# Kernel optimization log

Measured on AMD Instinct MI355X. Metric: run time of the kernel, lower is better.

## Reference

```python
import jax, jax.numpy as jnp
import numpy as np

N_NODES = 50000
NEG_SLOPE = 0.2


def gat_conv(x, W, att_src, att_dst, b, src, dst, n):
    # x: [N, F_in], W: [F_in, H*C], att_*: [H, C], b: [H*C]
    H, C = att_src.shape
    h = (x @ W).reshape(n, H, C)                       # [N, H, C]
    a_s = (h * att_src).sum(-1)                        # [N, H]
    a_d = (h * att_dst).sum(-1)                        # [N, H]
    e = jax.nn.leaky_relu(a_s[src] + a_d[dst], NEG_SLOPE)  # [E, H]
    # segment softmax over destination node (every node has a self-loop)
    m = jax.ops.segment_max(e, dst, num_segments=n)    # [N, H]
    ex = jnp.exp(e - m[dst])
    denom = jax.ops.segment_sum(ex, dst, num_segments=n)
    alpha = ex / denom[dst]                            # [E, H]
    out = jax.ops.segment_sum(alpha[:, :, None] * h[src], dst, num_segments=n)
    return out.reshape(n, H * C) + b


def setup_inputs() -> dict:
    key = jax.random.key(0)
    ks = jax.random.split(key, 10)
    n, e = N_NODES, 1600000
    x = jax.random.normal(ks[0], (n, 128), dtype=jnp.float32)
    edge_index = jax.random.randint(ks[1], (2, e), 0, n, dtype=jnp.int64)
    s = 0.1
    return {
        "x": x,
        "edge_index": edge_index,
        "W1": jax.random.normal(ks[2], (128, 128), dtype=jnp.float32) * s,
        "att_src1": jax.random.normal(ks[3], (4, 32), dtype=jnp.float32) * s,
        "att_dst1": jax.random.normal(ks[4], (4, 32), dtype=jnp.float32) * s,
        "b1": jnp.zeros((128,), dtype=jnp.float32),
        "W2": jax.random.normal(ks[5], (128, 128), dtype=jnp.float32) * s,
        "att_src2": jax.random.normal(ks[6], (4, 32), dtype=jnp.float32) * s,
        "att_dst2": jax.random.normal(ks[7], (4, 32), dtype=jnp.float32) * s,
        "b2": jnp.zeros((128,), dtype=jnp.float32),
    }


def reference(x, edge_index, W1, att_src1, att_dst1, b1, W2, att_src2, att_dst2, b2):
    n = x.shape[0]
    loops = jnp.arange(n, dtype=edge_index.dtype)
    src = jnp.concatenate([edge_index[0], loops])  # add self-loops (PyG default)
    dst = jnp.concatenate([edge_index[1], loops])
    h = gat_conv(x, W1, att_src1, att_dst1, b1, src, dst, n)
    h = jax.nn.relu(h)
    h = gat_conv(h, W2, att_src2, att_dst2, b2, src, dst, n)
    return (h, h)
```

## Files before the change

### kernel.cpp

```cpp
#include <hip/hip_runtime.h>
#include <hip/hip_bf16.h>


#define FDIM 128
#define NHEAD 4
#define NB 512

__device__ inline unsigned short f2bf(float f) {
    union { float f; unsigned u; } v; v.f = f;
    unsigned r = v.u + 0x7fff + ((v.u >> 16) & 1);
    return (unsigned short)(r >> 16);
}
__device__ inline float2 bf2f(unsigned v) {
    union { unsigned u; float f; } a, b;
    a.u = v << 16;
    b.u = v & 0xffff0000u;
    return make_float2(a.f, b.f);
}

__global__ __launch_bounds__(256) void gemm128(const float* __restrict__ A,
                                               const float* __restrict__ B,
                                               unsigned short* __restrict__ C,
                                               const float* __restrict__ att_s,
                                               const float* __restrict__ att_d,
                                               float* __restrict__ a_s,
                                               float* __restrict__ a_d, int M) {
    __shared__ float As[128 * 64];
    __shared__ float Bs[128 * 128];
    const int tid = threadIdx.x;
    const int bm = blockIdx.x * 64;

    #pragma unroll
    for (int i = 0; i < 16; i++) {
        int idx = tid + i * 256;
        ((float4*)Bs)[idx] = ((const float4*)B)[idx];
    }
    #pragma unroll
    for (int i = 0; i < 8; i++) {
        int idx = tid + i * 256;
        int row = idx >> 5;
        int k4  = idx & 31;
        int grow = bm + row;
        float4 v = make_float4(0.f, 0.f, 0.f, 0.f);
        if (grow < M) v = ((const float4*)A)[grow * 32 + k4];
        As[(k4 * 4 + 0) * 64 + row] = v.x;
        As[(k4 * 4 + 1) * 64 + row] = v.y;
        As[(k4 * 4 + 2) * 64 + row] = v.z;
        As[(k4 * 4 + 3) * 64 + row] = v.w;
    }
    __syncthreads();

    const int mg = tid >> 5;
    const int ng = tid & 31;
    float acc[8][4] = {};
    const float* Ap = &As[mg * 8];
    const float* Bp = &Bs[ng * 4];
    #pragma unroll 4
    for (int k = 0; k < 128; k++) {
        float4 a0 = *(const float4*)(Ap + k * 64);
        float4 a1 = *(const float4*)(Ap + k * 64 + 4);
        float4 b  = *(const float4*)(Bp + k * 128);
        float av[8] = {a0.x, a0.y, a0.z, a0.w, a1.x, a1.y, a1.z, a1.w};
        float bv[4] = {b.x, b.y, b.z, b.w};
        #pragma unroll
        for (int i = 0; i < 8; i++)
            #pragma unroll
            for (int j = 0; j < 4; j++)
                acc[i][j] += av[i] * bv[j];
    }

    const float4 atS = ((const float4*)att_s)[ng];
    const float4 atD = ((const float4*)att_d)[ng];
    #pragma unroll
    for (int i = 0; i < 8; i++) {
        int grow = bm + mg * 8 + i;
        float ps = acc[i][0] * atS.x + acc[i][1] * atS.y + acc[i][2] * atS.z + acc[i][3] * atS.w;
        float pd = acc[i][0] * atD.x + acc[i][1] * atD.y + acc[i][2] * atD.z + acc[i][3] * atD.w;
        ps += __shfl_xor(ps, 1, 64); pd += __shfl_xor(pd, 1, 64);
        ps += __shfl_xor(ps, 2, 64); pd += __shfl_xor(pd, 2, 64);
        ps += __shfl_xor(ps, 4, 64); pd += __shfl_xor(pd, 4, 64);
        if (grow < M) {
            ((ushort4*)C)[grow * 32 + ng] =
                make_ushort4(f2bf(acc[i][0]), f2bf(acc[i][1]),
                             f2bf(acc[i][2]), f2bf(acc[i][3]));
            if ((ng & 7) == 0) {
                a_s[grow * NHEAD + (ng >> 3)] = ps;
                a_d[grow * NHEAD + (ng >> 3)] = pd;
            }
        }
    }
}

__global__ __launch_bounds__(256) void bucket_hist(const int* __restrict__ dst, int E,
                                                   unsigned long long magic,
                                                   int* __restrict__ bcnt) {
    __shared__ int sh[NB];
    const int t = threadIdx.x;
    for (int i = t; i < NB; i += 256) sh[i] = 0;
    __syncthreads();
    for (int i = blockIdx.x * blockDim.x + t; i < E; i += gridDim.x * blockDim.x) {
        int b = (int)(((unsigned long long)(unsigned)dst[i] * magic) >> 40);
        atomicAdd(&sh[b], 1);
    }
    __syncthreads();
    for (int i = t; i < NB; i += 256)
        if (sh[i]) atomicAdd(&bcnt[i], sh[i]);
}

__global__ __launch_bounds__(256) void bucket_scan(const int* __restrict__ bcnt,
                                                   int* __restrict__ bbase,
                                                   int* __restrict__ bcursor,
                                                   int* __restrict__ row_ptr,
                                                   int N, int E) {
    __shared__ int wsum[4];
    const int t = threadIdx.x, lane = t & 63, wid = t >> 6;
    int v0 = bcnt[2 * t], v1 = bcnt[2 * t + 1];
    int s = v0 + v1, incl = s;
    #pragma unroll
    for (int o = 1; o < 64; o <<= 1) {
        int u = __shfl_up(incl, o, 64);
        if (lane >= o) incl += u;
    }
    if (lane == 63) wsum[wid] = incl;
    __syncthreads();
    if (t == 0) {
        int a = 0;
        #pragma unroll
        for (int i = 0; i < 4; i++) { int x = wsum[i]; wsum[i] = a; a += x; }
    }
    __syncthreads();
    int excl = wsum[wid] + incl - s;
    bbase[2 * t] = excl;          bcursor[2 * t] = excl;
    bbase[2 * t + 1] = excl + v0; bcursor[2 * t + 1] = excl + v0;
    if (t == 0) { bbase[NB] = E; row_ptr[N] = E; }
}

__global__ __launch_bounds__(256) void partition(const int* __restrict__ src,
                                                 const int* __restrict__ dst, int E,
                                                 unsigned long long magic,
                                                 int* __restrict__ bcursor,
                                                 int2* __restrict__ ebuf) {
    __shared__ int shc[NB];
    __shared__ int shb[NB];
    __shared__ int shcur[NB];
    const int t = threadIdx.x;
    for (int i = t; i < NB; i += 256) shc[i] = 0;
    __syncthreads();
    const int e0 = blockIdx.x * 4096;
    int myb[16], mys[16], myd[16];
    #pragma unroll
    for (int u = 0; u < 16; u++) {
        int i = e0 + u * 256 + t;
        if (i < E) {
            mys[u] = src[i];
            myd[u] = dst[i];
            int b = (int)(((unsigned long long)(unsigned)myd[u] * magic) >> 40);
            myb[u] = b;
            atomicAdd(&shc[b], 1);
        } else myb[u] = -1;
    }
    __syncthreads();
    for (int i = t; i < NB; i += 256) {
        int c = shc[i];
        shcur[i] = 0;
        if (c) shb[i] = atomicAdd(&bcursor[i], c);
    }
    __syncthreads();
    #pragma unroll
    for (int u = 0; u < 16; u++) {
        if (myb[u] >= 0) {
            int o = atomicAdd(&shcur[myb[u]], 1);
            ebuf[shb[myb[u]] + o] = make_int2(mys[u], myd[u]);
        }
    }
}

__global__ __launch_bounds__(256) void build_bucket(const int2* __restrict__ ebuf,
                                                    const int* __restrict__ bbase,
                                                    int npb, int N,
                                                    int* __restrict__ row_ptr,
                                                    int* __restrict__ col) {
    __shared__ int degl[256];
    __shared__ int curl[256];
    const int b = blockIdx.x;
    const int t = threadIdx.x, lane = t & 63, wid = t >> 6;
    const int base = bbase[b];
    const int cnt = bbase[b + 1] - base;
    const int node0 = b * npb;
    for (int i = t; i < npb; i += 256) degl[i] = 0;
    __syncthreads();
    for (int i = t; i < cnt; i += 256) {
        int d = ebuf[base + i].y;
        atomicAdd(&degl[d - node0], 1);
    }
    __syncthreads();
    if (wid == 0) {
        int run = 0;
        for (int c = 0; c * 64 < npb; c++) {
            int idx = c * 64 + lane;
            int v = (idx < npb) ? degl[idx] : 0;
            int incl = v;
            #pragma unroll
            for (int o = 1; o < 64; o <<= 1) {
                int u = __shfl_up(incl, o, 64);
                if (lane >= o) incl += u;
            }
            int excl = incl - v + run;
            if (idx < npb) {
                curl[idx] = excl;
                int node = node0 + idx;
                if (node < N) row_ptr[node] = base + excl;
            }
            run += __shfl(incl, 63, 64);
        }
    }
    __syncthreads();
    for (int i = t; i < cnt; i += 256) {
        int2 ed = ebuf[base + i];
        int p = atomicAdd(&curl[ed.y - node0], 1);
        col[base + p] = ed.x;
    }
}

__global__ __launch_bounds__(64) void aggregate(const unsigned short* __restrict__ h,
                                                const float* __restrict__ a_s,
                                                const float* __restrict__ a_d,
                                                const int* __restrict__ row_ptr,
                                                const int* __restrict__ col,
                                                const float* __restrict__ bias,
                                                float* __restrict__ out,
                                                float* __restrict__ out2,
                                                int n, int do_relu) {
    const int nid = blockIdx.x;
    const int c = threadIdx.x;
    const int hd = c >> 4;
    const float ad = a_d[nid * NHEAD + hd];
    const unsigned* __restrict__ h2 = (const unsigned*)h;

    float e = a_s[nid * NHEAD + hd] + ad;
    e = (e > 0.f) ? e : 0.2f * e;
    float den = __expf(e);
    float2 hv = bf2f(h2[(size_t)nid * 64 + c]);
    float num0 = den * hv.x, num1 = den * hv.y;

    const int beg = row_ptr[nid], end = row_ptr[nid + 1];
    int j = beg;
    for (; j + 8 <= end; j += 8) {
        int s[8];
        #pragma unroll
        for (int u = 0; u < 8; u++) s[u] = col[j + u];
        unsigned v[8]; float el[8];
        #pragma unroll
        for (int u = 0; u < 8; u++) v[u] = h2[(size_t)s[u] * 64 + c];
        #pragma unroll
        for (int u = 0; u < 8; u++) el[u] = a_s[s[u] * NHEAD + hd];
        #pragma unroll
        for (int u = 0; u < 8; u++) {
            float e2 = el[u] + ad;
            e2 = (e2 > 0.f) ? e2 : 0.2f * e2;
            float w = __expf(e2);
            den += w;
            float2 f = bf2f(v[u]);
            num0 += w * f.x;
            num1 += w * f.y;
        }
    }
    for (; j < end; j++) {
        int s = col[j];
        float e2 = a_s[s * NHEAD + hd] + ad;
        e2 = (e2 > 0.f) ? e2 : 0.2f * e2;
        float w = __expf(e2);
        den += w;
        float2 f = bf2f(h2[(size_t)s * 64 + c]);
        num0 += w * f.x;
        num1 += w * f.y;
    }
    float2 bv = ((const float2*)bias)[c];
    float rd = 1.0f / den;
    float o0 = num0 * rd + bv.x;
    float o1 = num1 * rd + bv.y;
    if (do_relu) { o0 = fmaxf(o0, 0.f); o1 = fmaxf(o1, 0.f); }
    ((float2*)out)[(size_t)nid * 64 + c] = make_float2(o0, o1);
    if (out2) ((float2*)out2)[(size_t)nid * 64 + c] = make_float2(o0, o1);
}

extern "C" void kernel_launch(void* const* d_in, const int* in_sizes, int n_in,
                              void* d_out, int out_size, void* d_ws, size_t ws_size,
                              hipStream_t stream) {
    const float* x        = (const float*)d_in[0];
    const int*   edge     = (const int*)d_in[1];
    const float* W1       = (const float*)d_in[2];
    const float* att_s1   = (const float*)d_in[3];
    const float* att_d1   = (const float*)d_in[4];
    const float* b1       = (const float*)d_in[5];
    const float* W2       = (const float*)d_in[6];
    const float* att_s2   = (const float*)d_in[7];
    const float* att_d2   = (const float*)d_in[8];
    const float* b2       = (const float*)d_in[9];
    float* out = (float*)d_out;

    const int N = in_sizes[0] / FDIM;
    const int E = in_sizes[1] / 2;
    const int* src = edge;
    const int* dst = edge + E;

    const int npb = (N + NB - 1) / NB;
    const unsigned long long magic = ((1ull << 40) / (unsigned long long)npb) + 1;

    char* w = (char*)d_ws;
    size_t off = 0;
    auto alloc = [&](size_t bytes) { void* p = w + off; off = (off + bytes + 255) & ~(size_t)255; return p; };
    int*   row_ptr = (int*)alloc((size_t)(N + 1) * 4);
    int*   col     = (int*)alloc((size_t)E * 4);
    int*   bcnt    = (int*)alloc((size_t)NB * 4);
    int*   bbase   = (int*)alloc((size_t)(NB + 1) * 4);
    int*   bcursor = (int*)alloc((size_t)NB * 4);
    unsigned short* h1 = (unsigned short*)alloc((size_t)N * FDIM * 2);
    float* hx      = (float*)alloc((size_t)N * FDIM * 4);
    float* as1     = (float*)alloc((size_t)N * NHEAD * 4);
    float* ad1     = (float*)alloc((size_t)N * NHEAD * 4);
    float* as2     = (float*)alloc((size_t)N * NHEAD * 4);
    float* ad2     = (float*)alloc((size_t)N * NHEAD * 4);
    int2*  ebuf    = (int2*)hx;
    (void)ws_size;

    hipMemsetAsync(bcnt, 0, (size_t)NB * 4, stream);
    bucket_hist<<<1024, 256, 0, stream>>>(dst, E, magic, bcnt);
    bucket_scan<<<1, 256, 0, stream>>>(bcnt, bbase, bcursor, row_ptr, N, E);
    partition<<<(E + 4095) / 4096, 256, 0, stream>>>(src, dst, E, magic, bcursor, ebuf);
    build_bucket<<<NB, 256, 0, stream>>>(ebuf, bbase, npb, N, row_ptr, col);

    const int gblocks = (N + 63) / 64;

    gemm128<<<gblocks, 256, 0, stream>>>(x, W1, h1, att_s1, att_d1, as1, ad1, N);
    aggregate<<<N, 64, 0, stream>>>(h1, as1, ad1, row_ptr, col, b1, hx, nullptr, N, 1);

    gemm128<<<gblocks, 256, 0, stream>>>(hx, W2, h1, att_s2, att_d2, as2, ad2, N);
    aggregate<<<N, 64, 0, stream>>>(h1, as2, ad2, row_ptr, col, b2,
                                    out, out + (size_t)N * FDIM, N, 0);
}
```

Before: 386.3 us.

## Replace FP32 SIMT GEMM with split-bf16 MFMA GEMM and fused attention dots

Replaces the scalar FP32 GEMM with a matrix-core kernel that splits each FP32 operand into bf16 hi and lo parts and issues three MFMA 32x32x16 products to approximate FP32 accuracy. The weights are pre-split and stored in LDS with an XOR swizzle by a small prep kernel, so B loads avoid bank conflicts. The output tile is staged through LDS for coalesced 16-byte stores, and the per-head attention dot products are recomputed there from the bf16 values. This trades slightly different numerics (the attention logits now come from rounded bf16 h) and two extra tiny launches for much higher GEMM throughput. The GEMMs are only part of the total time, which is dominated by graph building and aggregation.

```diff
diff --git a/kernel.cpp b/kernel.cpp
--- a/kernel.cpp
+++ b/kernel.cpp
@@ -5,6 +5,9 @@
 #define FDIM 128
 #define NHEAD 4
 #define NB 512
+
+typedef __attribute__((ext_vector_type(16))) float f32x16;
+typedef __attribute__((ext_vector_type(8)))  short s16x8;
 
 __device__ inline unsigned short f2bf(float f) {
     union { float f; unsigned u; } v; v.f = f;
@@ -18,75 +21,140 @@
     return make_float2(a.f, b.f);
 }
 
-__global__ __launch_bounds__(256) void gemm128(const float* __restrict__ A,
-                                               const float* __restrict__ B,
-                                               unsigned short* __restrict__ C,
-                                               const float* __restrict__ att_s,
-                                               const float* __restrict__ att_d,
-                                               float* __restrict__ a_s,
-                                               float* __restrict__ a_d, int M) {
-    __shared__ float As[128 * 64];
-    __shared__ float Bs[128 * 128];
-    const int tid = threadIdx.x;
+__global__ __launch_bounds__(256) void prep_w(const float* __restrict__ W,
+                                              short* __restrict__ Bhi,
+                                              short* __restrict__ Blo) {
+    const int t = threadIdx.x;
+    for (int i = 0; i < 64; i++) {
+        int e = i * 256 + t;
+        int k = e >> 7, n = e & 127;
+        float f = W[e];
+        unsigned u = __float_as_uint(f);
+        unsigned short hi = (unsigned short)(u >> 16);
+        float rem = f - __uint_as_float(u & 0xffff0000u);
+        unsigned short lo = (unsigned short)(__float_as_uint(rem) >> 16);
+        int idx = n * 128 + ((((k >> 3) ^ (n & 15))) << 3) + (k & 7);
+        Bhi[idx] = (short)hi;
+        Blo[idx] = (short)lo;
+    }
+}
+
+__global__ __launch_bounds__(256) void gemm_mfma(const float* __restrict__ A,
+                                                 const short* __restrict__ Bghi,
+                                                 const short* __restrict__ Bglo,
+                                                 unsigned short* __restrict__ H,
+                                                 const float* __restrict__ att_s,
+                                                 const float* __restrict__ att_d,
+                                                 float* __restrict__ a_s,
+                                                 float* __restrict__ a_d, int M) {
+    __shared__ short Bsm[2][16384];
+    __shared__ float attsm[256];
+    const int t = threadIdx.x;
     const int bm = blockIdx.x * 64;
 
-    #pragma unroll
-    for (int i = 0; i < 16; i++) {
-        int idx = tid + i * 256;
-        ((float4*)Bs)[idx] = ((const float4*)B)[idx];
-    }
-    #pragma unroll
-    for (int i = 0; i < 8; i++) {
-        int idx = tid + i * 256;
-        int row = idx >> 5;
-        int k4  = idx & 31;
-        int grow = bm + row;
-        float4 v = make_float4(0.f, 0.f, 0.f, 0.f);
-        if (grow < M) v = ((const float4*)A)[grow * 32 + k4];
-        As[(k4 * 4 + 0) * 64 + row] = v.x;
-        As[(k4 * 4 + 1) * 64 + row] = v.y;
-        As[(k4 * 4 + 2) * 64 + row] = v.z;
-        As[(k4 * 4 + 3) * 64 + row] = v.w;
-    }
-    __syncthreads();
-
-    const int mg = tid >> 5;
-    const int ng = tid & 31;
-    float acc[8][4] = {};
-    const float* Ap = &As[mg * 8];
-    const float* Bp = &Bs[ng * 4];
-    #pragma unroll 4
-    for (int k = 0; k < 128; k++) {
-        float4 a0 = *(const float4*)(Ap + k * 64);
-        float4 a1 = *(const float4*)(Ap + k * 64 + 4);
-        float4 b  = *(const float4*)(Bp + k * 128);
-        float av[8] = {a0.x, a0.y, a0.z, a0.w, a1.x, a1.y, a1.z, a1.w};
-        float bv[4] = {b.x, b.y, b.z, b.w};
-        #pragma unroll
-        for (int i = 0; i < 8; i++)
+    if (t < 128) attsm[t] = att_s[t];
+    else         attsm[t] = att_d[t - 128];
+
+    {
+        const uint4* ghi = (const uint4*)Bghi;
+        const uint4* glo = (const uint4*)Bglo;
+        uint4* shi = (uint4*)&Bsm[0][0];
+        uint4* slo = (uint4*)&Bsm[1][0];
+        #pragma unroll
+        for (int i = 0; i < 8; i++) {
+            shi[t + i * 256] = ghi[t + i * 256];
+            slo[t + i * 256] = glo[t + i * 256];
+        }
+    }
+
+    const int lane = t & 63;
+    const int w = t >> 6;
+    const int wr = w >> 1, wc = w & 1;
+    const int m  = lane & 31, h2 = lane >> 5;
+    const int grow = bm + wr * 32 + m;
+
+    s16x8 ahi[8], alo[8];
+    {
+        const bool ok = grow < M;
+        const float* ap = A + (size_t)grow * 128 + 8 * h2;
+        #pragma unroll
+        for (int c = 0; c < 8; c++) {
+            float ff[8];
+            if (ok) {
+                float4 f0 = *(const float4*)(ap + c * 16);
+                float4 f1 = *(const float4*)(ap + c * 16 + 4);
+                ff[0]=f0.x; ff[1]=f0.y; ff[2]=f0.z; ff[3]=f0.w;
+                ff[4]=f1.x; ff[5]=f1.y; ff[6]=f1.z; ff[7]=f1.w;
+            } else {
+                #pragma unroll
+                for (int j = 0; j < 8; j++) ff[j] = 0.f;
+            }
             #pragma unroll
-            for (int j = 0; j < 4; j++)
-                acc[i][j] += av[i] * bv[j];
-    }
-
-    const float4 atS = ((const float4*)att_s)[ng];
-    const float4 atD = ((const float4*)att_d)[ng];
-    #pragma unroll
-    for (int i = 0; i < 8; i++) {
-        int grow = bm + mg * 8 + i;
-        float ps = acc[i][0] * atS.x + acc[i][1] * atS.y + acc[i][2] * atS.z + acc[i][3] * atS.w;
-        float pd = acc[i][0] * atD.x + acc[i][1] * atD.y + acc[i][2] * atD.z + acc[i][3] * atD.w;
-        ps += __shfl_xor(ps, 1, 64); pd += __shfl_xor(pd, 1, 64);
-        ps += __shfl_xor(ps, 2, 64); pd += __shfl_xor(pd, 2, 64);
-        ps += __shfl_xor(ps, 4, 64); pd += __shfl_xor(pd, 4, 64);
-        if (grow < M) {
-            ((ushort4*)C)[grow * 32 + ng] =
-                make_ushort4(f2bf(acc[i][0]), f2bf(acc[i][1]),
-                             f2bf(acc[i][2]), f2bf(acc[i][3]));
-            if ((ng & 7) == 0) {
-                a_s[grow * NHEAD + (ng >> 3)] = ps;
-                a_d[grow * NHEAD + (ng >> 3)] = pd;
+            for (int j = 0; j < 8; j++) {
+                unsigned u = __float_as_uint(ff[j]);
+                float rem = ff[j] - __uint_as_float(u & 0xffff0000u);
+                ahi[c][j] = (short)(u >> 16);
+                alo[c][j] = (short)(__float_as_uint(rem) >> 16);
             }
+        }
+    }
+    __syncthreads();
+
+    f32x16 acc[2];
+    #pragma unroll
+    for (int i = 0; i < 16; i++) { acc[0][i] = 0.f; acc[1][i] = 0.f; }
+
+    #pragma unroll
+    for (int ni = 0; ni < 2; ni++) {
+        const int n = ni * 64 + wc * 32 + m;
+        const int nbase = n * 128;
+        #pragma unroll
+        for (int c = 0; c < 8; c++) {
+            int chunk8 = 2 * c + h2;
+            int koff = ((chunk8 ^ (n & 15)) << 3);
+            s16x8 bhi = *(const s16x8*)&Bsm[0][nbase + koff];
+            s16x8 blo = *(const s16x8*)&Bsm[1][nbase + koff];
+            acc[ni] = __builtin_amdgcn_mfma_f32_32x32x16_bf16(ahi[c], bhi, acc[ni], 0, 0, 0);
+            acc[ni] = __builtin_amdgcn_mfma_f32_32x32x16_bf16(alo[c], bhi, acc[ni], 0, 0, 0);
+            acc[ni] = __builtin_amdgcn_mfma_f32_32x32x16_bf16(ahi[c], blo, acc[ni], 0, 0, 0);
+        }
+    }
+
+    __syncthreads();
+    unsigned short* htile = (unsigned short*)&Bsm[0][0];
+    #pragma unroll
+    for (int ni = 0; ni < 2; ni++) {
+        const int colg = ni * 64 + wc * 32 + m;
+        #pragma unroll
+        for (int r = 0; r < 16; r++) {
+            int row = wr * 32 + (r & 3) + 8 * (r >> 2) + 4 * h2;
+            htile[row * 128 + colg] = (short)f2bf(acc[ni][r]);
+        }
+    }
+    __syncthreads();
+
+    {
+        const int r = t >> 2, q = t & 3;
+        const int growr = bm + r;
+        if (growr < M) {
+            uint4 v0 = *(uint4*)&htile[r * 128 + q * 32];
+            uint4 v1 = *(uint4*)&htile[r * 128 + q * 32 + 8];
+            uint4 v2 = *(uint4*)&htile[r * 128 + q * 32 + 16];
+            uint4 v3 = *(uint4*)&htile[r * 128 + q * 32 + 24];
+            uint4* hg = (uint4*)(H + (size_t)growr * 128);
+            hg[q * 4 + 0] = v0; hg[q * 4 + 1] = v1;
+            hg[q * 4 + 2] = v2; hg[q * 4 + 3] = v3;
+            unsigned uu[16] = {v0.x, v0.y, v0.z, v0.w, v1.x, v1.y, v1.z, v1.w,
+                               v2.x, v2.y, v2.z, v2.w, v3.x, v3.y, v3.z, v3.w};
+            float ps = 0.f, pd = 0.f;
+            #pragma unroll
+            for (int i = 0; i < 16; i++) {
+                float2 f = bf2f(uu[i]);
+                ps += f.x * attsm[q * 32 + 2 * i]       + f.y * attsm[q * 32 + 2 * i + 1];
+                pd += f.x * attsm[128 + q * 32 + 2 * i] + f.y * attsm[128 + q * 32 + 2 * i + 1];
+            }
+            a_s[growr * NHEAD + q] = ps;
+            a_d[growr * NHEAD + q] = pd;
         }
     }
 }
@@ -258,22 +326,22 @@
         for (int u = 0; u < 8; u++) {
             float e2 = el[u] + ad;
             e2 = (e2 > 0.f) ? e2 : 0.2f * e2;
-            float w = __expf(e2);
-            den += w;
+            float wgt = __expf(e2);
+            den += wgt;
             float2 f = bf2f(v[u]);
-            num0 += w * f.x;
-            num1 += w * f.y;
+            num0 += wgt * f.x;
+            num1 += wgt * f.y;
         }
     }
     for (; j < end; j++) {
         int s = col[j];
         float e2 = a_s[s * NHEAD + hd] + ad;
         e2 = (e2 > 0.f) ? e2 : 0.2f * e2;
-        float w = __expf(e2);
-        den += w;
+        float wgt = __expf(e2);
+        den += wgt;
         float2 f = bf2f(h2[(size_t)s * 64 + c]);
-        num0 += w * f.x;
-        num1 += w * f.y;
+        num0 += wgt * f.x;
+        num1 += wgt * f.y;
     }
     float2 bv = ((const float2*)bias)[c];
     float rd = 1.0f / den;
@@ -321,8 +389,15 @@
     float* ad1     = (float*)alloc((size_t)N * NHEAD * 4);
     float* as2     = (float*)alloc((size_t)N * NHEAD * 4);
     float* ad2     = (float*)alloc((size_t)N * NHEAD * 4);
+    short* Bg1hi   = (short*)alloc((size_t)128 * 128 * 2);
+    short* Bg1lo   = (short*)alloc((size_t)128 * 128 * 2);
+    short* Bg2hi   = (short*)alloc((size_t)128 * 128 * 2);
+    short* Bg2lo   = (short*)alloc((size_t)128 * 128 * 2);
     int2*  ebuf    = (int2*)hx;
     (void)ws_size;
+
+    prep_w<<<1, 256, 0, stream>>>(W1, Bg1hi, Bg1lo);
+    prep_w<<<1, 256, 0, stream>>>(W2, Bg2hi, Bg2lo);
 
     hipMemsetAsync(bcnt, 0, (size_t)NB * 4, stream);
     bucket_hist<<<1024, 256, 0, stream>>>(dst, E, magic, bcnt);
@@ -332,10 +407,10 @@
 
     const int gblocks = (N + 63) / 64;
 
-    gemm128<<<gblocks, 256, 0, stream>>>(x, W1, h1, att_s1, att_d1, as1, ad1, N);
+    gemm_mfma<<<gblocks, 256, 0, stream>>>(x, Bg1hi, Bg1lo, h1, att_s1, att_d1, as1, ad1, N);
     aggregate<<<N, 64, 0, stream>>>(h1, as1, ad1, row_ptr, col, b1, hx, nullptr, N, 1);
 
-    gemm128<<<gblocks, 256, 0, stream>>>(hx, W2, h1, att_s2, att_d2, as2, ad2, N);
+    gemm_mfma<<<gblocks, 256, 0, stream>>>(hx, Bg2hi, Bg2lo, h1, att_s2, att_d2, as2, ad2, N);
     aggregate<<<N, 64, 0, stream>>>(h1, as2, ad2, row_ptr, col, b2,
                                     out, out + (size_t)N * FDIM, N, 0);
 }
```

Result: faster. 348.6 us (-9.8%).
